# Kernel tuning notes

Hardware: AMD Instinct MI355X
Metric: run time of the kernel (lower is better)

The kernel has to match this reference:

```python
import jax, jax.numpy as jnp
import numpy as np
from jax import lax

GAMMA = 0.1


def setup_inputs() -> dict:
    key = jax.random.key(0)
    k1, k2 = jax.random.split(key)
    pred = jax.random.normal(k1, (64, 512), dtype=jnp.float32)
    target = jax.random.normal(k2, (64, 512), dtype=jnp.float32)
    return {"pred": pred, "target": target}


def _soft_dtw(pred, target, gamma=GAMMA):
    # pred, target: [B, L]
    B, L = pred.shape
    inf = jnp.float32(jnp.inf)
    # pairwise squared distances: [B, L, L]
    dist = (pred[:, :, None] - target[:, None, :]) ** 2

    def softmin3(r0, r1, r2):
        # -gamma * logsumexp(-r/gamma) over the 3 predecessors (stable)
        s = jnp.stack([r0, r1, r2], axis=-1)
        return -gamma * jax.nn.logsumexp(-s / gamma, axis=-1)

    # R[0, :] = [0, inf, inf, ...]  (row 0 of the (L+1)x(L+1) DP table)
    init_row = jnp.concatenate(
        [jnp.zeros((B, 1), jnp.float32), jnp.full((B, L), inf, jnp.float32)], axis=1
    )  # [B, L+1]

    def row_step(prev_row, d_row):
        # prev_row: R[i-1, :] of shape [B, L+1]; d_row: dist[:, i-1, :] of shape [B, L]
        r0s = prev_row[:, :-1].T  # R[i-1, j-1], [L, B]
        r1s = prev_row[:, 1:].T   # R[i-1, j],   [L, B]
        ds = d_row.T              # [L, B]

        def cell(r_left, inp):
            r0, r1, d = inp
            val = d + softmin3(r0, r1, r_left)
            return val, val

        _, vals = lax.scan(cell, jnp.full((B,), inf, jnp.float32), (r0s, r1s, ds))
        new_row = jnp.concatenate([jnp.full((B, 1), inf, jnp.float32), vals.T], axis=1)
        return new_row, None

    # scan over rows i = 1..L; dist reordered to [L, B, L]
    last_row, _ = lax.scan(row_step, init_row, jnp.swapaxes(dist, 0, 1))
    return last_row[:, -1].mean()  # R[:, L, L].mean()


def reference(pred, target):
    return _soft_dtw(pred, target)
```

## Files before the change

kernel.cpp:

```cpp
#include <hip/hip_runtime.h>

#define LSEQ 512
#define NB 64
#define NCHUNK 51

__device__ __forceinline__ float dpp_shr1(float old, float x) {
  return __int_as_float(__builtin_amdgcn_update_dpp(
      __float_as_int(old), __float_as_int(x), 0x138, 0xF, 0xF, false));
}
__device__ __forceinline__ float dpp_shl1(float x) {
  return __int_as_float(__builtin_amdgcn_update_dpp(
      0, __float_as_int(x), 0x130, 0xF, 0xF, false));
}

__device__ __forceinline__ void renorm(float& d, float& e) {
  const int eb = __float_as_int(e);
  const int E = (eb >> 23) - 127;
  e = __int_as_float((eb & 0x007FFFFF) | 0x3F800000);
  d -= (float)E;
}

template <bool FULL>
__device__ __forceinline__ void chunk16(
    int cbase, const float* tg, const float2* ring2P, float2* ring2W, float p0,
    float p1, bool is_wr, int lane, float& v0d, float& v0e, float& v1d,
    float& v1e, float& r0d, float& r0e, float& tcur) {
  renorm(v0d, v0e);
  renorm(v1d, v1e);

  float tinj = tg[(cbase + (lane & 15)) & 511];
  const float2 rj = ring2P[(cbase + 1 + (lane & 15)) & 127];
  float rdinj = rj.x, reinj = rj.y;

  float2 vv[16];
#pragma unroll
  for (int u = 0; u < 16; ++u) {
    tcur = dpp_shr1(tinj, tcur);
    const float r1d = dpp_shr1(rdinj, v1d);
    const float r1e = dpp_shr1(reinj, v1e);
    if (u < 15) {
      tinj = dpp_shl1(tinj);
      rdinj = dpp_shl1(rdinj);
      reinj = dpp_shl1(reinj);
    }
    const float diff0 = p0 - tcur;
    const float M0 = fminf(fminf(r0d, r1d), v0d);
    const float e0 = (__builtin_amdgcn_exp2f(M0 - r0d) * r0e +
                      __builtin_amdgcn_exp2f(M0 - r1d) * r1e) +
                     __builtin_amdgcn_exp2f(M0 - v0d) * v0e;
    const float d0 = __builtin_fmaf(diff0, diff0, M0);
    const float diff1 = p1 - tcur;
    const float M1 = fminf(fminf(v0d, d0), v1d);
    const float e1 = (__builtin_amdgcn_exp2f(M1 - v0d) * v0e +
                      __builtin_amdgcn_exp2f(M1 - d0) * e0) +
                     __builtin_amdgcn_exp2f(M1 - v1d) * v1e;
    const float d1 = __builtin_fmaf(diff1, diff1, M1);
    vv[u] = make_float2(d1, e1);
    if (FULL) {
      v0d = d0; v0e = e0; v1d = d1; v1e = e1;
    } else {
      const int j = cbase + 1 + u - lane;
      const bool act = ((unsigned)(j - 1)) < (unsigned)LSEQ;
      v0d = act ? d0 : v0d; v0e = act ? e0 : v0e;
      v1d = act ? d1 : v1d; v1e = act ? e1 : v1e;
    }
    r0d = r1d;
    r0e = r1e;
  }

  if (is_wr) {
    const int j0 = cbase - 62;
#pragma unroll
    for (int k = 0; k < 16; ++k) {
      if (FULL || (((unsigned)(j0 + k - 1)) < (unsigned)LSEQ))
        ring2W[(j0 + k) & 127] = vv[k];
    }
  }
}

__global__ __launch_bounds__(256) void dtw_band(
    const float* __restrict__ pred, const float* __restrict__ target,
    float* __restrict__ part) {
  const int b = blockIdx.x;
  const int tid = threadIdx.x;
  const int w = tid >> 6;
  const int lane = tid & 63;
  const bool is_wr = (lane == 63) && (w < 3);

  __shared__ float tg[LSEQ];
  __shared__ float2 rings2[4][128];

  const float SC = 3.79828146f;
  const float2 pp = ((const float2*)(pred + b * LSEQ))[tid];
  const float p0 = pp.x * SC, p1 = pp.y * SC;
  const float2 tt = ((const float2*)(target + b * LSEQ))[tid];
  ((float2*)tg)[tid] = make_float2(tt.x * SC, tt.y * SC);
  ((float2*)rings2)[tid] = make_float2(INFINITY, 1.0f);
  ((float2*)rings2)[tid + 256] = make_float2(INFINITY, 1.0f);

  const int lag = w * 80;
  const int cw0 = 5 * w;
  const float2* __restrict__ ring2P = rings2[w == 0 ? 3 : w - 1];
  float2* __restrict__ ring2W = rings2[w];

  float v0d = INFINITY, v0e = 1.0f;
  float v1d = INFINITY, v1e = 1.0f;
  float r0d = (tid == 0) ? 0.0f : INFINITY;
  float r0e = 1.0f;
  float tcur = 0.0f;

  for (int c = 0; c < NCHUNK; ++c) {
    __syncthreads();
    if (c < cw0 || c > cw0 + 35) continue;
    const int cbase = 16 * c - lag;
    if (c >= cw0 + 4 && c <= cw0 + 31)
      chunk16<true>(cbase, tg, ring2P, ring2W, p0, p1, is_wr, lane, v0d, v0e,
                    v1d, v1e, r0d, r0e, tcur);
    else
      chunk16<false>(cbase, tg, ring2P, ring2W, p0, p1, is_wr, lane, v0d, v0e,
                     v1d, v1e, r0d, r0e, tcur);
  }

  if (tid == 255)
    part[b] = (v1d - __builtin_amdgcn_logf(v1e)) * 0.069314718f;
}

__global__ void dtw_reduce(const float* __restrict__ part,
                           float* __restrict__ out) {
  float v = part[threadIdx.x];
#pragma unroll
  for (int o = 32; o > 0; o >>= 1) v += __shfl_down(v, o);
  if (threadIdx.x == 0) out[0] = v * (1.0f / NB);
}

extern "C" void kernel_launch(void* const* d_in, const int* in_sizes, int n_in,
                              void* d_out, int out_size, void* d_ws,
                              size_t ws_size, hipStream_t stream) {
  const float* pred = (const float*)d_in[0];
  const float* target = (const float*)d_in[1];
  float* part = (float*)d_ws;

  dtw_band<<<NB, 256, 0, stream>>>(pred, target, part);
  dtw_reduce<<<1, 64, 0, stream>>>(part, (float*)d_out);
}
```

Before: 90.28 us.

## Process four rows per thread with two waves per batch block

Each thread now computes four consecutive DP rows instead of two, so a batch element uses two waves (128 threads) instead of four. This shortens the wavefront pipeline (fewer chunks and barriers) and halves the shared ring buffers. In exchange each step carries a longer serial chain of dependent cells, and the block has fewer waves to hide latency.

```diff
diff --git a/kernel.cpp b/kernel.cpp
--- a/kernel.cpp
+++ b/kernel.cpp
@@ -2,7 +2,7 @@
 
 #define LSEQ 512
 #define NB 64
-#define NCHUNK 51
+#define NCHUNK 41
 
 __device__ __forceinline__ float dpp_shr1(float old, float x) {
   return __int_as_float(__builtin_amdgcn_update_dpp(
@@ -20,49 +20,60 @@
   d -= (float)E;
 }
 
+__device__ __forceinline__ void cell(float p, float t, float ad, float ae,
+                                     float bd, float be, float cd, float ce,
+                                     float& od, float& oe) {
+  const float diff = p - t;
+  const float M = fminf(fminf(ad, bd), cd);
+  oe = (__builtin_amdgcn_exp2f(M - ad) * ae +
+        __builtin_amdgcn_exp2f(M - bd) * be) +
+       __builtin_amdgcn_exp2f(M - cd) * ce;
+  od = __builtin_fmaf(diff, diff, M);
+}
+
 template <bool FULL>
 __device__ __forceinline__ void chunk16(
-    int cbase, const float* tg, const float2* ring2P, float2* ring2W, float p0,
-    float p1, bool is_wr, int lane, float& v0d, float& v0e, float& v1d,
-    float& v1e, float& r0d, float& r0e, float& tcur) {
+    int cbase, const float* tg, const float2* ring2P, float2* ring2W,
+    float p0, float p1, float p2, float p3, bool is_wr, int lane, float& v0d,
+    float& v0e, float& v1d, float& v1e, float& v2d, float& v2e, float& v3d,
+    float& v3e, float& r0d, float& r0e, float& tcur) {
   renorm(v0d, v0e);
   renorm(v1d, v1e);
+  renorm(v2d, v2e);
+  renorm(v3d, v3e);
 
   float tinj = tg[(cbase + (lane & 15)) & 511];
   const float2 rj = ring2P[(cbase + 1 + (lane & 15)) & 127];
   float rdinj = rj.x, reinj = rj.y;
 
-  float2 vv[16];
+  float vvd[16], vve[16];
 #pragma unroll
   for (int u = 0; u < 16; ++u) {
     tcur = dpp_shr1(tinj, tcur);
-    const float r1d = dpp_shr1(rdinj, v1d);
-    const float r1e = dpp_shr1(reinj, v1e);
+    const float r1d = dpp_shr1(rdinj, v3d);
+    const float r1e = dpp_shr1(reinj, v3e);
     if (u < 15) {
       tinj = dpp_shl1(tinj);
       rdinj = dpp_shl1(rdinj);
       reinj = dpp_shl1(reinj);
     }
-    const float diff0 = p0 - tcur;
-    const float M0 = fminf(fminf(r0d, r1d), v0d);
-    const float e0 = (__builtin_amdgcn_exp2f(M0 - r0d) * r0e +
-                      __builtin_amdgcn_exp2f(M0 - r1d) * r1e) +
-                     __builtin_amdgcn_exp2f(M0 - v0d) * v0e;
-    const float d0 = __builtin_fmaf(diff0, diff0, M0);
-    const float diff1 = p1 - tcur;
-    const float M1 = fminf(fminf(v0d, d0), v1d);
-    const float e1 = (__builtin_amdgcn_exp2f(M1 - v0d) * v0e +
-                      __builtin_amdgcn_exp2f(M1 - d0) * e0) +
-                     __builtin_amdgcn_exp2f(M1 - v1d) * v1e;
-    const float d1 = __builtin_fmaf(diff1, diff1, M1);
-    vv[u] = make_float2(d1, e1);
+    float d0, e0, d1, e1, d2, e2, d3, e3;
+    cell(p0, tcur, r0d, r0e, r1d, r1e, v0d, v0e, d0, e0);
+    cell(p1, tcur, v0d, v0e, d0, e0, v1d, v1e, d1, e1);
+    cell(p2, tcur, v1d, v1e, d1, e1, v2d, v2e, d2, e2);
+    cell(p3, tcur, v2d, v2e, d2, e2, v3d, v3e, d3, e3);
+    vvd[u] = d3;
+    vve[u] = e3;
     if (FULL) {
       v0d = d0; v0e = e0; v1d = d1; v1e = e1;
+      v2d = d2; v2e = e2; v3d = d3; v3e = e3;
     } else {
       const int j = cbase + 1 + u - lane;
       const bool act = ((unsigned)(j - 1)) < (unsigned)LSEQ;
       v0d = act ? d0 : v0d; v0e = act ? e0 : v0e;
       v1d = act ? d1 : v1d; v1e = act ? e1 : v1e;
+      v2d = act ? d2 : v2d; v2e = act ? e2 : v2e;
+      v3d = act ? d3 : v3d; v3e = act ? e3 : v3e;
     }
     r0d = r1d;
     r0e = r1e;
@@ -73,38 +84,39 @@
 #pragma unroll
     for (int k = 0; k < 16; ++k) {
       if (FULL || (((unsigned)(j0 + k - 1)) < (unsigned)LSEQ))
-        ring2W[(j0 + k) & 127] = vv[k];
+        ring2W[(j0 + k) & 127] = make_float2(vvd[k], vve[k]);
     }
   }
 }
 
-__global__ __launch_bounds__(256) void dtw_band(
+__global__ __launch_bounds__(128) void dtw_band(
     const float* __restrict__ pred, const float* __restrict__ target,
     float* __restrict__ part) {
   const int b = blockIdx.x;
   const int tid = threadIdx.x;
   const int w = tid >> 6;
   const int lane = tid & 63;
-  const bool is_wr = (lane == 63) && (w < 3);
+  const bool is_wr = (lane == 63) && (w == 0);
 
   __shared__ float tg[LSEQ];
-  __shared__ float2 rings2[4][128];
+  __shared__ float2 rings2[2][128];
 
   const float SC = 3.79828146f;
-  const float2 pp = ((const float2*)(pred + b * LSEQ))[tid];
-  const float p0 = pp.x * SC, p1 = pp.y * SC;
-  const float2 tt = ((const float2*)(target + b * LSEQ))[tid];
-  ((float2*)tg)[tid] = make_float2(tt.x * SC, tt.y * SC);
+  const float4 pp = ((const float4*)(pred + b * LSEQ))[tid];
+  const float p0 = pp.x * SC, p1 = pp.y * SC, p2 = pp.z * SC, p3 = pp.w * SC;
+  const float4 tt = ((const float4*)(target + b * LSEQ))[tid];
+  ((float4*)tg)[tid] = make_float4(tt.x * SC, tt.y * SC, tt.z * SC, tt.w * SC);
   ((float2*)rings2)[tid] = make_float2(INFINITY, 1.0f);
-  ((float2*)rings2)[tid + 256] = make_float2(INFINITY, 1.0f);
+  ((float2*)rings2)[tid + 128] = make_float2(INFINITY, 1.0f);
 
-  const int lag = w * 80;
   const int cw0 = 5 * w;
-  const float2* __restrict__ ring2P = rings2[w == 0 ? 3 : w - 1];
-  float2* __restrict__ ring2W = rings2[w];
+  const float2* __restrict__ ring2P = rings2[w == 0 ? 1 : 0];
+  float2* __restrict__ ring2W = rings2[0];
 
   float v0d = INFINITY, v0e = 1.0f;
   float v1d = INFINITY, v1e = 1.0f;
+  float v2d = INFINITY, v2e = 1.0f;
+  float v3d = INFINITY, v3e = 1.0f;
   float r0d = (tid == 0) ? 0.0f : INFINITY;
   float r0e = 1.0f;
   float tcur = 0.0f;
@@ -112,17 +124,17 @@
   for (int c = 0; c < NCHUNK; ++c) {
     __syncthreads();
     if (c < cw0 || c > cw0 + 35) continue;
-    const int cbase = 16 * c - lag;
+    const int cbase = 16 * c - 80 * w;
     if (c >= cw0 + 4 && c <= cw0 + 31)
-      chunk16<true>(cbase, tg, ring2P, ring2W, p0, p1, is_wr, lane, v0d, v0e,
-                    v1d, v1e, r0d, r0e, tcur);
+      chunk16<true>(cbase, tg, ring2P, ring2W, p0, p1, p2, p3, is_wr, lane,
+                    v0d, v0e, v1d, v1e, v2d, v2e, v3d, v3e, r0d, r0e, tcur);
     else
-      chunk16<false>(cbase, tg, ring2P, ring2W, p0, p1, is_wr, lane, v0d, v0e,
-                     v1d, v1e, r0d, r0e, tcur);
+      chunk16<false>(cbase, tg, ring2P, ring2W, p0, p1, p2, p3, is_wr, lane,
+                     v0d, v0e, v1d, v1e, v2d, v2e, v3d, v3e, r0d, r0e, tcur);
   }
 
-  if (tid == 255)
-    part[b] = (v1d - __builtin_amdgcn_logf(v1e)) * 0.069314718f;
+  if (tid == 127)
+    part[b] = (v3d - __builtin_amdgcn_logf(v3e)) * 0.069314718f;
 }
 
 __global__ void dtw_reduce(const float* __restrict__ part,
@@ -140,6 +152,6 @@
   const float* target = (const float*)d_in[1];
   float* part = (float*)d_ws;
 
-  dtw_band<<<NB, 256, 0, stream>>>(pred, target, part);
+  dtw_band<<<NB, 128, 0, stream>>>(pred, target, part);
   dtw_reduce<<<1, 64, 0, stream>>>(part, (float*)d_out);
 }
```

Result: slower. 106.8 us (+18.3%).

## Process two batch items per block to interleave independent DP chains

Applied to the files above, without the earlier changes.

Each block now computes two independent soft-DTW problems (A and B), interleaving their per-cell steps so the two dependency chains can hide each other's exp and DPP latency. The grid is halved to 32 blocks, and the exp-weighted sums are rewritten as FMA chains. The cost is more registers and LDS per block, plus fewer blocks, so only about an eighth of the GPU's compute units get work; the per-block serial length is unchanged, so any gain has to come from instruction-level parallelism.

```diff
diff --git a/kernel.cpp b/kernel.cpp
--- a/kernel.cpp
+++ b/kernel.cpp
@@ -20,60 +20,87 @@
   d -= (float)E;
 }
 
+struct St {
+  float v0d, v0e, v1d, v1e;
+  float r0d, r0e;
+  float tcur;
+  float p0, p1;
+};
+
+template <bool FULL>
+__device__ __forceinline__ void step_one(int cbase, int u, const float* tg,
+                                         const float2* ring2P, St& s,
+                                         float& tinj, float& rdinj,
+                                         float& reinj, int lane, float& outd,
+                                         float& oute) {
+  s.tcur = dpp_shr1(tinj, s.tcur);
+  const float r1d = dpp_shr1(rdinj, s.v1d);
+  const float r1e = dpp_shr1(reinj, s.v1e);
+  if (u < 15) {
+    tinj = dpp_shl1(tinj);
+    rdinj = dpp_shl1(rdinj);
+    reinj = dpp_shl1(reinj);
+  }
+  const float diff0 = s.p0 - s.tcur;
+  const float M0 = fminf(fminf(s.r0d, r1d), s.v0d);
+  const float d0 = __builtin_fmaf(diff0, diff0, M0);
+  const float diff1 = s.p1 - s.tcur;
+  const float M1 = fminf(fminf(s.v0d, d0), s.v1d);
+  const float d1 = __builtin_fmaf(diff1, diff1, M1);
+  const float x0 = __builtin_amdgcn_exp2f(M0 - s.r0d);
+  const float x1 = __builtin_amdgcn_exp2f(M0 - r1d);
+  const float x2 = __builtin_amdgcn_exp2f(M0 - s.v0d);
+  const float x3 = __builtin_amdgcn_exp2f(M1 - s.v0d);
+  const float x4 = __builtin_amdgcn_exp2f(M1 - d0);
+  const float x5 = __builtin_amdgcn_exp2f(M1 - s.v1d);
+  const float e0 = __builtin_fmaf(x2, s.v0e, __builtin_fmaf(x1, r1e, x0 * s.r0e));
+  const float e1 = __builtin_fmaf(x5, s.v1e, __builtin_fmaf(x4, e0, x3 * s.v0e));
+  outd = d1;
+  oute = e1;
+  if (FULL) {
+    s.v0d = d0; s.v0e = e0; s.v1d = d1; s.v1e = e1;
+  } else {
+    const int j = cbase + 1 + u - lane;
+    const bool act = ((unsigned)(j - 1)) < (unsigned)LSEQ;
+    s.v0d = act ? d0 : s.v0d; s.v0e = act ? e0 : s.v0e;
+    s.v1d = act ? d1 : s.v1d; s.v1e = act ? e1 : s.v1e;
+  }
+  s.r0d = r1d;
+  s.r0e = r1e;
+}
+
 template <bool FULL>
 __device__ __forceinline__ void chunk16(
-    int cbase, const float* tg, const float2* ring2P, float2* ring2W, float p0,
-    float p1, bool is_wr, int lane, float& v0d, float& v0e, float& v1d,
-    float& v1e, float& r0d, float& r0e, float& tcur) {
-  renorm(v0d, v0e);
-  renorm(v1d, v1e);
+    int cbase, const float* tgA, const float* tgB, const float2* ringPA,
+    float2* ringWA, const float2* ringPB, float2* ringWB, bool is_wr, int lane,
+    St& A, St& B) {
+  renorm(A.v0d, A.v0e); renorm(A.v1d, A.v1e);
+  renorm(B.v0d, B.v0e); renorm(B.v1d, B.v1e);
 
-  float tinj = tg[(cbase + (lane & 15)) & 511];
-  const float2 rj = ring2P[(cbase + 1 + (lane & 15)) & 127];
-  float rdinj = rj.x, reinj = rj.y;
+  float tinjA = tgA[(cbase + (lane & 15)) & 511];
+  const float2 rjA = ringPA[(cbase + 1 + (lane & 15)) & 127];
+  float rdinjA = rjA.x, reinjA = rjA.y;
+  float tinjB = tgB[(cbase + (lane & 15)) & 511];
+  const float2 rjB = ringPB[(cbase + 1 + (lane & 15)) & 127];
+  float rdinjB = rjB.x, reinjB = rjB.y;
 
-  float2 vv[16];
+  float vvdA[16], vveA[16], vvdB[16], vveB[16];
 #pragma unroll
   for (int u = 0; u < 16; ++u) {
-    tcur = dpp_shr1(tinj, tcur);
-    const float r1d = dpp_shr1(rdinj, v1d);
-    const float r1e = dpp_shr1(reinj, v1e);
-    if (u < 15) {
-      tinj = dpp_shl1(tinj);
-      rdinj = dpp_shl1(rdinj);
-      reinj = dpp_shl1(reinj);
-    }
-    const float diff0 = p0 - tcur;
-    const float M0 = fminf(fminf(r0d, r1d), v0d);
-    const float e0 = (__builtin_amdgcn_exp2f(M0 - r0d) * r0e +
-                      __builtin_amdgcn_exp2f(M0 - r1d) * r1e) +
-                     __builtin_amdgcn_exp2f(M0 - v0d) * v0e;
-    const float d0 = __builtin_fmaf(diff0, diff0, M0);
-    const float diff1 = p1 - tcur;
-    const float M1 = fminf(fminf(v0d, d0), v1d);
-    const float e1 = (__builtin_amdgcn_exp2f(M1 - v0d) * v0e +
-                      __builtin_amdgcn_exp2f(M1 - d0) * e0) +
-                     __builtin_amdgcn_exp2f(M1 - v1d) * v1e;
-    const float d1 = __builtin_fmaf(diff1, diff1, M1);
-    vv[u] = make_float2(d1, e1);
-    if (FULL) {
-      v0d = d0; v0e = e0; v1d = d1; v1e = e1;
-    } else {
-      const int j = cbase + 1 + u - lane;
-      const bool act = ((unsigned)(j - 1)) < (unsigned)LSEQ;
-      v0d = act ? d0 : v0d; v0e = act ? e0 : v0e;
-      v1d = act ? d1 : v1d; v1e = act ? e1 : v1e;
-    }
-    r0d = r1d;
-    r0e = r1e;
+    step_one<FULL>(cbase, u, tgA, ringPA, A, tinjA, rdinjA, reinjA, lane,
+                   vvdA[u], vveA[u]);
+    step_one<FULL>(cbase, u, tgB, ringPB, B, tinjB, rdinjB, reinjB, lane,
+                   vvdB[u], vveB[u]);
   }
 
   if (is_wr) {
     const int j0 = cbase - 62;
 #pragma unroll
     for (int k = 0; k < 16; ++k) {
-      if (FULL || (((unsigned)(j0 + k - 1)) < (unsigned)LSEQ))
-        ring2W[(j0 + k) & 127] = vv[k];
+      if (FULL || (((unsigned)(j0 + k - 1)) < (unsigned)LSEQ)) {
+        ringWA[(j0 + k) & 127] = make_float2(vvdA[k], vveA[k]);
+        ringWB[(j0 + k) & 127] = make_float2(vvdB[k], vveB[k]);
+      }
     }
   }
 }
@@ -87,42 +114,54 @@
   const int lane = tid & 63;
   const bool is_wr = (lane == 63) && (w < 3);
 
-  __shared__ float tg[LSEQ];
-  __shared__ float2 rings2[4][128];
+  __shared__ float tgA[LSEQ], tgB[LSEQ];
+  __shared__ float2 ringsA[4][128], ringsB[4][128];
 
   const float SC = 3.79828146f;
-  const float2 pp = ((const float2*)(pred + b * LSEQ))[tid];
-  const float p0 = pp.x * SC, p1 = pp.y * SC;
-  const float2 tt = ((const float2*)(target + b * LSEQ))[tid];
-  ((float2*)tg)[tid] = make_float2(tt.x * SC, tt.y * SC);
-  ((float2*)rings2)[tid] = make_float2(INFINITY, 1.0f);
-  ((float2*)rings2)[tid + 256] = make_float2(INFINITY, 1.0f);
+  St A, B;
+  {
+    const float2 ppA = ((const float2*)(pred + (2 * b) * LSEQ))[tid];
+    A.p0 = ppA.x * SC; A.p1 = ppA.y * SC;
+    const float2 ttA = ((const float2*)(target + (2 * b) * LSEQ))[tid];
+    ((float2*)tgA)[tid] = make_float2(ttA.x * SC, ttA.y * SC);
+    const float2 ppB = ((const float2*)(pred + (2 * b + 1) * LSEQ))[tid];
+    B.p0 = ppB.x * SC; B.p1 = ppB.y * SC;
+    const float2 ttB = ((const float2*)(target + (2 * b + 1) * LSEQ))[tid];
+    ((float2*)tgB)[tid] = make_float2(ttB.x * SC, ttB.y * SC);
+    ((float2*)ringsA)[tid] = make_float2(INFINITY, 1.0f);
+    ((float2*)ringsA)[tid + 256] = make_float2(INFINITY, 1.0f);
+    ((float2*)ringsB)[tid] = make_float2(INFINITY, 1.0f);
+    ((float2*)ringsB)[tid + 256] = make_float2(INFINITY, 1.0f);
+  }
 
   const int lag = w * 80;
   const int cw0 = 5 * w;
-  const float2* __restrict__ ring2P = rings2[w == 0 ? 3 : w - 1];
-  float2* __restrict__ ring2W = rings2[w];
+  const float2* __restrict__ ringPA = ringsA[w == 0 ? 3 : w - 1];
+  float2* __restrict__ ringWA = ringsA[w];
+  const float2* __restrict__ ringPB = ringsB[w == 0 ? 3 : w - 1];
+  float2* __restrict__ ringWB = ringsB[w];
 
-  float v0d = INFINITY, v0e = 1.0f;
-  float v1d = INFINITY, v1e = 1.0f;
-  float r0d = (tid == 0) ? 0.0f : INFINITY;
-  float r0e = 1.0f;
-  float tcur = 0.0f;
+  A.v0d = INFINITY; A.v0e = 1.0f; A.v1d = INFINITY; A.v1e = 1.0f;
+  A.r0d = (tid == 0) ? 0.0f : INFINITY; A.r0e = 1.0f; A.tcur = 0.0f;
+  B.v0d = INFINITY; B.v0e = 1.0f; B.v1d = INFINITY; B.v1e = 1.0f;
+  B.r0d = (tid == 0) ? 0.0f : INFINITY; B.r0e = 1.0f; B.tcur = 0.0f;
 
   for (int c = 0; c < NCHUNK; ++c) {
     __syncthreads();
     if (c < cw0 || c > cw0 + 35) continue;
     const int cbase = 16 * c - lag;
     if (c >= cw0 + 4 && c <= cw0 + 31)
-      chunk16<true>(cbase, tg, ring2P, ring2W, p0, p1, is_wr, lane, v0d, v0e,
-                    v1d, v1e, r0d, r0e, tcur);
+      chunk16<true>(cbase, tgA, tgB, ringPA, ringWA, ringPB, ringWB, is_wr,
+                    lane, A, B);
     else
-      chunk16<false>(cbase, tg, ring2P, ring2W, p0, p1, is_wr, lane, v0d, v0e,
-                     v1d, v1e, r0d, r0e, tcur);
+      chunk16<false>(cbase, tgA, tgB, ringPA, ringWA, ringPB, ringWB, is_wr,
+                     lane, A, B);
   }
 
-  if (tid == 255)
-    part[b] = (v1d - __builtin_amdgcn_logf(v1e)) * 0.069314718f;
+  if (tid == 255) {
+    part[2 * b] = (A.v1d - __builtin_amdgcn_logf(A.v1e)) * 0.069314718f;
+    part[2 * b + 1] = (B.v1d - __builtin_amdgcn_logf(B.v1e)) * 0.069314718f;
+  }
 }
 
 __global__ void dtw_reduce(const float* __restrict__ part,
@@ -140,6 +179,6 @@
   const float* target = (const float*)d_in[1];
   float* part = (float*)d_ws;
 
-  dtw_band<<<NB, 256, 0, stream>>>(pred, target, part);
+  dtw_band<<<NB / 2, 256, 0, stream>>>(pred, target, part);
   dtw_reduce<<<1, 64, 0, stream>>>(part, (float*)d_out);
 }
```

New measurement: 157.4 us. 1.74x slower.
